# Kernel optimization log

Measured on AMD Instinct MI355X. Metric: run time of the kernel, lower is better.

The kernel has to match this reference:

```python
import jax, jax.numpy as jnp
import numpy as np

EPS = 1e-5

def _conv(x, w, b, groups=1, pad=0):
    # x: NCHW, w: OIHW (I = in_ch/groups)
    y = jax.lax.conv_general_dilated(
        x, w, window_strides=(1, 1), padding=[(pad, pad), (pad, pad)],
        feature_group_count=groups,
        dimension_numbers=('NCHW', 'OIHW', 'NCHW'))
    return y + b[None, :, None, None]

def _bn(x, g, b, m, v):
    scale = g * jax.lax.rsqrt(v + EPS)
    return x * scale[None, :, None, None] + (b - m * scale)[None, :, None, None]

def _block(x, w_dw, b_dw, w_pw, b_pw, g, b, m, v, groups):
    h = _conv(x, w_dw, b_dw, groups=groups, pad=1)   # 3x3 grouped conv
    h = _conv(h, w_pw, b_pw)                          # 1x1 pointwise 2C->C
    return jax.nn.relu(_bn(h, g, b, m, v))

def setup_inputs() -> dict:
    key = jax.random.key(0)
    ks = jax.random.split(key, 16)
    B, C, H, W = 4, 256, 64, 64
    s = 0.02  # small weight scale to keep softmax logits well-conditioned
    return {
        'x1': jax.random.normal(ks[0], (B, C, H, W), jnp.float32),
        'x2': jax.random.normal(ks[1], (B, C, H, W), jnp.float32),
        'w1_dw': jax.random.normal(ks[2], (2 * C, 2, 3, 3), jnp.float32) * s,
        'b1_dw': jnp.zeros((2 * C,), jnp.float32),
        'w1_pw': jax.random.normal(ks[3], (C, 2 * C, 1, 1), jnp.float32) * s,
        'b1_pw': jnp.zeros((C,), jnp.float32),
        'bn1_g': jnp.ones((C,), jnp.float32),
        'bn1_b': jnp.zeros((C,), jnp.float32),
        'bn1_m': jnp.zeros((C,), jnp.float32),
        'bn1_v': jnp.ones((C,), jnp.float32),
        'w2_dw': jax.random.normal(ks[4], (2 * C, 2, 3, 3), jnp.float32) * s,
        'b2_dw': jnp.zeros((2 * C,), jnp.float32),
        'w2_pw': jax.random.normal(ks[5], (C, 2 * C, 1, 1), jnp.float32) * s,
        'b2_pw': jnp.zeros((C,), jnp.float32),
        'bn2_g': jnp.ones((C,), jnp.float32),
        'bn2_b': jnp.zeros((C,), jnp.float32),
        'bn2_m': jnp.zeros((C,), jnp.float32),
        'bn2_v': jnp.ones((C,), jnp.float32),
        'wq': jax.random.normal(ks[6], (C // 8, C, 1, 1), jnp.float32) * s,
        'bq': jnp.zeros((C // 8,), jnp.float32),
        'wk': jax.random.normal(ks[7], (C // 8, C, 1, 1), jnp.float32) * s,
        'bk': jnp.zeros((C // 8,), jnp.float32),
        'wv': jax.random.normal(ks[8], (C, C, 1, 1), jnp.float32) * s,
        'bv': jnp.zeros((C,), jnp.float32),
        'gamma': jnp.ones((1,), jnp.float32),
    }

def reference(x1, x2,
              w1_dw, b1_dw, w1_pw, b1_pw, bn1_g, bn1_b, bn1_m, bn1_v,
              w2_dw, b2_dw, w2_pw, b2_pw, bn2_g, bn2_b, bn2_m, bn2_v,
              wq, bq, wk, bk, wv, bv, gamma):
    B, C, H, W = x1.shape
    N = H * W
    sub = x1 - x2
    concat1 = jnp.concatenate([sub, x1], axis=1)  # [B,2C,H,W]
    concat2 = jnp.concatenate([sub, x2], axis=1)
    x3 = _block(concat1, w1_dw, b1_dw, w1_pw, b1_pw, bn1_g, bn1_b, bn1_m, bn1_v, groups=C)
    x4 = _block(concat2, w2_dw, b2_dw, w2_pw, b2_pw, bn2_g, bn2_b, bn2_m, bn2_v, groups=C)
    q = _conv(x4, wq, bq).reshape(B, -1, N)   # [B, C//8, N]
    k = _conv(x3, wk, bk).reshape(B, -1, N)   # [B, C//8, N]
    v = _conv(x3, wv, bv).reshape(B, C, N)    # [B, C, N]
    energy = jnp.einsum('bdq,bdk->bqk', q, k)          # [B, N, N]
    attn = jax.nn.softmax(energy, axis=-1)
    out = jnp.einsum('bck,bqk->bcq', v, attn)          # [B, C, N]
    out = out.reshape(B, C, H, W)
    return gamma[0] * out + x1
```

## Files before the change

### kernel.cpp

```cpp
#include <hip/hip_runtime.h>
#include <hip/hip_bf16.h>

#define EPSB 1e-5f

typedef __hip_bfloat16 bf16;
typedef __attribute__((ext_vector_type(8))) short bf16x8;
typedef __attribute__((ext_vector_type(4))) float f32x4;

__device__ __forceinline__ unsigned short f2bu(float x) {
  bf16 h = __float2bfloat16(x);
  return *reinterpret_cast<unsigned short*>(&h);
}
__device__ __forceinline__ unsigned int pk2(float lo, float hi) {
  return ((unsigned int)f2bu(hi) << 16) | (unsigned int)f2bu(lo);
}

__global__ __launch_bounds__(256) void k_dwconv3(
    const float* __restrict__ x1, const float* __restrict__ x2,
    const float* __restrict__ w1, const float* __restrict__ b1,
    const float* __restrict__ w2, const float* __restrict__ b2,
    const float* __restrict__ w1pw, const float* __restrict__ w2pw,
    bf16* __restrict__ h1, bf16* __restrict__ h2,
    bf16* __restrict__ o1, bf16* __restrict__ o2) {
  if (blockIdx.y == 4) {
    int x = blockIdx.x;
    if (x < 128) {
      int i = (x * 256 + threadIdx.x) * 4;
      float4 a = *(const float4*)(w1pw + i);
      float4 c = *(const float4*)(w2pw + i);
      uint2 ua = {pk2(a.x, a.y), pk2(a.z, a.w)};
      uint2 uc = {pk2(c.x, c.y), pk2(c.z, c.w)};
      *(uint2*)&o1[i] = ua;
      *(uint2*)&o2[i] = uc;
    }
    return;
  }

  __shared__ float img[2 * 64 * 64];
  int g = blockIdx.x, b = blockIdx.y;
  int t = threadIdx.x;
  int row = t >> 2, x0 = (t & 3) * 16;
  bool xlo = (x0 == 0), xhi = (x0 == 48);
  size_t obase = (((size_t)(b * 512 + 2 * g)) << 12) + row * 64 + x0;

  auto stencil = [&](const float* wp, float bs0, float bs1, bf16* hout) {
    float o0[16], o1v[16];
#pragma unroll
    for (int i = 0; i < 16; i++) { o0[i] = bs0; o1v[i] = bs1; }
#pragma unroll
    for (int ch = 0; ch < 2; ch++) {
      float wa[9], wb[9];
#pragma unroll
      for (int i = 0; i < 9; i++) { wa[i] = wp[ch * 9 + i]; wb[i] = wp[18 + ch * 9 + i]; }
      const float* ib = img + ch * 4096;
#pragma unroll
      for (int ky = 0; ky < 3; ky++) {
        int yy = row + ky - 1;
        if (yy < 0 || yy > 63) continue;
        const float* rp = ib + yy * 64 + x0;
        float v[18];
        v[0] = xlo ? 0.f : rp[-1];
#pragma unroll
        for (int c = 1; c < 17; c++) v[c] = rp[c - 1];
        v[17] = xhi ? 0.f : rp[16];
        float a0 = wa[ky * 3], a1 = wa[ky * 3 + 1], a2 = wa[ky * 3 + 2];
        float c0 = wb[ky * 3], c1 = wb[ky * 3 + 1], c2 = wb[ky * 3 + 2];
#pragma unroll
        for (int i = 0; i < 16; i++) {
          o0[i] += a0 * v[i] + a1 * v[i + 1] + a2 * v[i + 2];
          o1v[i] += c0 * v[i] + c1 * v[i + 1] + c2 * v[i + 2];
        }
      }
    }
    uint4 u0 = {pk2(o0[0], o0[1]), pk2(o0[2], o0[3]), pk2(o0[4], o0[5]), pk2(o0[6], o0[7])};
    uint4 u1 = {pk2(o0[8], o0[9]), pk2(o0[10], o0[11]), pk2(o0[12], o0[13]), pk2(o0[14], o0[15])};
    *(uint4*)&hout[obase] = u0;
    *(uint4*)&hout[obase + 8] = u1;
    uint4 w0 = {pk2(o1v[0], o1v[1]), pk2(o1v[2], o1v[3]), pk2(o1v[4], o1v[5]), pk2(o1v[6], o1v[7])};
    uint4 w1v = {pk2(o1v[8], o1v[9]), pk2(o1v[10], o1v[11]), pk2(o1v[12], o1v[13]), pk2(o1v[14], o1v[15])};
    *(uint4*)&hout[obase + 4096] = w0;
    *(uint4*)&hout[obase + 4096 + 8] = w1v;
  };

  if (g < 128) {
    const float4* p1 = (const float4*)(x1 + ((size_t)(b * 256 + 2 * g) << 12));
    const float4* p2 = (const float4*)(x2 + ((size_t)(b * 256 + 2 * g) << 12));
#pragma unroll
    for (int u = 0; u < 8; u++) {
      int i = u * 256 + t;
      float4 a = p1[i], c = p2[i];
      float4 d = {a.x - c.x, a.y - c.y, a.z - c.z, a.w - c.w};
      ((float4*)img)[i] = d;
    }
  } else {
    const float4* p1 = (const float4*)(x1 + ((size_t)(b * 256 + 2 * (g - 128)) << 12));
#pragma unroll
    for (int u = 0; u < 8; u++) {
      int i = u * 256 + t;
      ((float4*)img)[i] = p1[i];
    }
  }
  __syncthreads();
  stencil(w1 + (size_t)(2 * g) * 18, b1[2 * g], b1[2 * g + 1], h1);

  if (g >= 128) {
    __syncthreads();
    const float4* p2 = (const float4*)(x2 + ((size_t)(b * 256 + 2 * (g - 128)) << 12));
#pragma unroll
    for (int u = 0; u < 8; u++) {
      int i = u * 256 + t;
      ((float4*)img)[i] = p2[i];
    }
    __syncthreads();
  }
  stencil(w2 + (size_t)(2 * g) * 18, b2[2 * g], b2[2 * g + 1], h2);
}

__global__ __launch_bounds__(256) void k_gemm_pw2(
    const bf16* __restrict__ In1, const bf16* __restrict__ In2,
    const bf16* __restrict__ W1, const bf16* __restrict__ W2,
    const float* __restrict__ bias1, const float* __restrict__ bias2,
    const float* __restrict__ g1v, const float* __restrict__ be1,
    const float* __restrict__ m1v, const float* __restrict__ v1v,
    const float* __restrict__ g2v, const float* __restrict__ be2,
    const float* __restrict__ m2v, const float* __restrict__ v2v,
    bf16* __restrict__ Out1, bf16* __restrict__ Out2) {
  __shared__ __align__(16) bf16 Al[128][40];
  __shared__ __align__(16) bf16 Bl[128][40];

  int lin = (blockIdx.z * 2 + blockIdx.y) * 32 + blockIdx.x;
  int xcd = lin & 7, slot = lin >> 3;
  int sel = xcd >> 2, b = xcd & 3;
  int p0 = (slot & 31) * 128;
  int oc0 = (slot >> 5) * 128;

  const bf16* In    = sel ? In2 : In1;
  const bf16* W     = sel ? W2 : W1;
  const float* bias = sel ? bias2 : bias1;
  const float* bng  = sel ? g2v : g1v;
  const float* bnb  = sel ? be2 : be1;
  const float* bnm  = sel ? m2v : m1v;
  const float* bnv  = sel ? v2v : v1v;
  bf16* Out         = sel ? Out2 : Out1;

  int t = threadIdx.x;
  int w = t >> 6, lane = t & 63, l16 = lane & 15, quad = lane >> 4;
  int wr = w >> 1, wc = w & 1;
  const bf16* Inb = In + (size_t)b * 512 * 4096;

  f32x4 acc[4][4];
#pragma unroll
  for (int mi = 0; mi < 4; mi++)
#pragma unroll
    for (int nj = 0; nj < 4; nj++) acc[mi][nj] = (f32x4){0.f, 0.f, 0.f, 0.f};

  int ocl = t >> 1, kb = (t & 1) * 16;
  int sch = t >> 3, soct = sch >> 3, swi = sch & 7, spg = t & 7;

  for (int kc = 0; kc < 512; kc += 32) {
    __syncthreads();
    {
      const bf16* src = W + (size_t)(oc0 + ocl) * 512 + kc + kb;
      uint4 u0 = *(const uint4*)(src);
      uint4 u1 = *(const uint4*)(src + 8);
      *(uint4*)&Al[ocl][kb] = u0;
      *(uint4*)&Al[ocl][kb + 8] = u1;
    }
    {
      const bf16* src = Inb + (size_t)(kc + sch) * 4096 + p0 + spg * 16;
      uint4 qv0 = *(const uint4*)src;
      uint4 qv1 = *(const uint4*)(src + 8);
      const unsigned short* qs0 = (const unsigned short*)&qv0;
      const unsigned short* qs1 = (const unsigned short*)&qv1;
#pragma unroll
      for (int j = 0; j < 8; j++) {
        int pix = spg * 16 + j;
        int col = (((soct ^ (pix >> 3)) & 3) << 3) | swi;
        *(unsigned short*)&Bl[pix][col] = qs0[j];
      }
#pragma unroll
      for (int j = 0; j < 8; j++) {
        int pix = spg * 16 + 8 + j;
        int col = (((soct ^ (pix >> 3)) & 3) << 3) | swi;
        *(unsigned short*)&Bl[pix][col] = qs1[j];
      }
    }
    __syncthreads();
    bf16x8 af[4], bv[4];
#pragma unroll
    for (int mi = 0; mi < 4; mi++)
      af[mi] = *(const bf16x8*)&Al[wr * 64 + mi * 16 + l16][quad * 8];
#pragma unroll
    for (int nj = 0; nj < 4; nj++) {
      int s = (nj * 2 + (l16 >> 3)) & 3;
      bv[nj] = *(const bf16x8*)&Bl[wc * 64 + nj * 16 + l16][(quad ^ s) * 8];
    }
#pragma unroll
    for (int mi = 0; mi < 4; mi++)
#pragma unroll
      for (int nj = 0; nj < 4; nj++)
        acc[mi][nj] = __builtin_amdgcn_mfma_f32_16x16x32_bf16(
            af[mi], bv[nj], acc[mi][nj], 0, 0, 0);
  }

#pragma unroll
  for (int mi = 0; mi < 4; mi++) {
    int ocb = oc0 + wr * 64 + mi * 16 + quad * 4;
    float4 bs4 = *(const float4*)&bias[ocb];
    float4 g4 = *(const float4*)&bng[ocb];
    float4 b4 = *(const float4*)&bnb[ocb];
    float4 m4 = *(const float4*)&bnm[ocb];
    float4 v4 = *(const float4*)&bnv[ocb];
    float sc[4], sh[4];
    sc[0] = g4.x * rsqrtf(v4.x + EPSB); sh[0] = bs4.x * sc[0] + b4.x - m4.x * sc[0];
    sc[1] = g4.y * rsqrtf(v4.y + EPSB); sh[1] = bs4.y * sc[1] + b4.y - m4.y * sc[1];
    sc[2] = g4.z * rsqrtf(v4.z + EPSB); sh[2] = bs4.z * sc[2] + b4.z - m4.z * sc[2];
    sc[3] = g4.w * rsqrtf(v4.w + EPSB); sh[3] = bs4.w * sc[3] + b4.w - m4.w * sc[3];
#pragma unroll
    for (int nj = 0; nj < 4; nj++) {
      int p = p0 + wc * 64 + nj * 16 + l16;
#pragma unroll
      for (int r = 0; r < 4; r++) {
        float val = fmaxf(acc[mi][nj][r] * sc[r] + sh[r], 0.f);
        Out[(((size_t)(b * 256 + ocb + r)) << 12) + p] = __float2bfloat16(val);
      }
    }
  }
}

__global__ __launch_bounds__(256) void k_gemm_qkv(
    const bf16* __restrict__ x3, const bf16* __restrict__ x4,
    const float* __restrict__ wv, const float* __restrict__ bv,
    const float* __restrict__ wq, const float* __restrict__ wk,
    const float* __restrict__ bq, const float* __restrict__ bk,
    bf16* __restrict__ vvb, bf16* __restrict__ qbf, bf16* __restrict__ kbf) {
  __shared__ __align__(16) bf16 Al[128][40];
  __shared__ __align__(16) bf16 Bl[128][40];

  int lin = (blockIdx.z * 2 + blockIdx.y) * 96 + blockIdx.x;
  int xcd = lin & 7, slot = lin >> 3;
  int b = xcd >> 1;
  int idx = ((xcd & 1) * 96) + slot;
  int by = idx / 96;
  int bx = idx % 96;

  int t = threadIdx.x;
  int w = t >> 6, lane = t & 63, l16 = lane & 15, quad = lane >> 4;
  int sch = t >> 3, soct = sch >> 3, swi = sch & 7, spg = t & 7;

  if (bx < 64) {
    int wr = w >> 1, wc = w & 1;
    int p0 = bx * 64;
    int oc0 = by * 128;
    const bf16* Inb = x3 + (size_t)b * 256 * 4096;

    f32x4 acc[4][2];
#pragma unroll
    for (int mi = 0; mi < 4; mi++)
#pragma unroll
      for (int nj = 0; nj < 2; nj++) acc[mi][nj] = (f32x4){0.f, 0.f, 0.f, 0.f};

    int ocl = t >> 1, kb = (t & 1) * 16;

    for (int kc = 0; kc < 256; kc += 32) {
      __syncthreads();
      {
        const float* src = wv + (size_t)(oc0 + ocl) * 256 + kc + kb;
        float4 f0 = *(const float4*)(src);
        float4 f1 = *(const float4*)(src + 4);
        float4 f2 = *(const float4*)(src + 8);
        float4 f3 = *(const float4*)(src + 12);
        uint4 u0 = {pk2(f0.x, f0.y), pk2(f0.z, f0.w), pk2(f1.x, f1.y), pk2(f1.z, f1.w)};
        uint4 u1 = {pk2(f2.x, f2.y), pk2(f2.z, f2.w), pk2(f3.x, f3.y), pk2(f3.z, f3.w)};
        *(uint4*)&Al[ocl][kb] = u0;
        *(uint4*)&Al[ocl][kb + 8] = u1;
      }
      {
        const bf16* src = Inb + (size_t)(kc + sch) * 4096 + p0 + spg * 8;
        uint4 qv = *(const uint4*)src;
        const unsigned short* qs = (const unsigned short*)&qv;
#pragma unroll
        for (int j = 0; j < 8; j++) {
          int pix = spg * 8 + j;
          int col = (((soct ^ (pix >> 3)) & 3) << 3) | swi;
          *(unsigned short*)&Bl[pix][col] = qs[j];
        }
      }
      __syncthreads();
      bf16x8 af[4], bvv[2];
#pragma unroll
      for (int mi = 0; mi < 4; mi++)
        af[mi] = *(const bf16x8*)&Al[wr * 64 + mi * 16 + l16][quad * 8];
#pragma unroll
      for (int nj = 0; nj < 2; nj++) {
        int s = (nj * 2 + (l16 >> 3)) & 3;
        bvv[nj] = *(const bf16x8*)&Bl[wc * 32 + nj * 16 + l16][(quad ^ s) * 8];
      }
#pragma unroll
      for (int mi = 0; mi < 4; mi++)
#pragma unroll
        for (int nj = 0; nj < 2; nj++)
          acc[mi][nj] = __builtin_amdgcn_mfma_f32_16x16x32_bf16(
              af[mi], bvv[nj], acc[mi][nj], 0, 0, 0);
    }

#pragma unroll
    for (int mi = 0; mi < 4; mi++) {
      int ocb = oc0 + wr * 64 + mi * 16 + quad * 4;
      float4 bs4 = *(const float4*)&bv[ocb];
      float sh[4] = {bs4.x, bs4.y, bs4.z, bs4.w};
#pragma unroll
      for (int nj = 0; nj < 2; nj++) {
        int p = p0 + wc * 32 + nj * 16 + l16;
#pragma unroll
        for (int r = 0; r < 4; r++) {
          float val = acc[mi][nj][r] + sh[r];
          vvb[(((size_t)(b * 256 + ocb + r)) << 12) + p] = __float2bfloat16(val);
        }
      }
    }
  } else {
    int p0 = (bx - 64) * 128;
    const bf16* In  = (by == 0) ? x4 : x3;
    const float* W  = (by == 0) ? wq : wk;
    const float* bi = (by == 0) ? bq : bk;
    bf16* Out       = (by == 0) ? qbf : kbf;
    const bf16* Inb = In + (size_t)b * 256 * 4096;

    f32x4 acc[2][2];
#pragma unroll
    for (int mi = 0; mi < 2; mi++)
#pragma unroll
      for (int nj = 0; nj < 2; nj++) acc[mi][nj] = (f32x4){0.f, 0.f, 0.f, 0.f};

    int aocl = t >> 3, akb = (t & 7) * 4;

    for (int kc = 0; kc < 256; kc += 32) {
      __syncthreads();
      {
        const float* src = W + (size_t)aocl * 256 + kc + akb;
        float4 f0 = *(const float4*)(src);
        uint2 u = {pk2(f0.x, f0.y), pk2(f0.z, f0.w)};
        *(uint2*)&Al[aocl][akb] = u;
      }
      {
        const bf16* src = Inb + (size_t)(kc + sch) * 4096 + p0 + spg * 16;
        uint4 qv0 = *(const uint4*)src;
        uint4 qv1 = *(const uint4*)(src + 8);
        const unsigned short* qs0 = (const unsigned short*)&qv0;
        const unsigned short* qs1 = (const unsigned short*)&qv1;
#pragma unroll
        for (int j = 0; j < 8; j++) {
          int pix = spg * 16 + j;
          int col = (((soct ^ (pix >> 3)) & 3) << 3) | swi;
          *(unsigned short*)&Bl[pix][col] = qs0[j];
        }
#pragma unroll
        for (int j = 0; j < 8; j++) {
          int pix = spg * 16 + 8 + j;
          int col = (((soct ^ (pix >> 3)) & 3) << 3) | swi;
          *(unsigned short*)&Bl[pix][col] = qs1[j];
        }
      }
      __syncthreads();
      bf16x8 af[2], bvv[2];
#pragma unroll
      for (int mi = 0; mi < 2; mi++)
        af[mi] = *(const bf16x8*)&Al[mi * 16 + l16][quad * 8];
#pragma unroll
      for (int nj = 0; nj < 2; nj++) {
        int s = (nj * 2 + (l16 >> 3)) & 3;
        bvv[nj] = *(const bf16x8*)&Bl[w * 32 + nj * 16 + l16][(quad ^ s) * 8];
      }
#pragma unroll
      for (int mi = 0; mi < 2; mi++)
#pragma unroll
        for (int nj = 0; nj < 2; nj++)
          acc[mi][nj] = __builtin_amdgcn_mfma_f32_16x16x32_bf16(
              af[mi], bvv[nj], acc[mi][nj], 0, 0, 0);
    }

#pragma unroll
    for (int mi = 0; mi < 2; mi++) {
      int ocb = mi * 16 + quad * 4;
      float4 bs4 = *(const float4*)&bi[ocb];
      float bs[4] = {bs4.x, bs4.y, bs4.z, bs4.w};
#pragma unroll
      for (int nj = 0; nj < 2; nj++) {
        int p = p0 + w * 32 + nj * 16 + l16;
        float v0 = acc[mi][nj][0] + bs[0];
        float v1 = acc[mi][nj][1] + bs[1];
        float v2 = acc[mi][nj][2] + bs[2];
        float v3 = acc[mi][nj][3] + bs[3];
        uint2 u = {pk2(v0, v1), pk2(v2, v3)};
        *(uint2*)&Out[((size_t)(b * 4096) + p) * 32 + ocb] = u;
      }
    }
  }
}

__global__ __launch_bounds__(512, 4) void k_attn_mfma(
    const bf16* __restrict__ qb, const bf16* __restrict__ kb,
    const bf16* __restrict__ vb, const float* __restrict__ x1,
    const float* __restrict__ gamma, float* __restrict__ out) {
  __shared__ __align__(16) bf16 Pl[2][64 * 128];
  __shared__ float lsumw[8][64];

  int t = threadIdx.x;
  int w = t >> 6, lane = t & 63;
  int l16 = lane & 15, quad = lane >> 4;

  int lin = blockIdx.y * 128 + blockIdx.x;
  int xcd = lin & 7, slot = lin >> 3;
  int b = xcd >> 1;
  int chalf = xcd & 1;
  int q0 = slot * 64;

  const bf16* kbb = kb + (size_t)b * 4096 * 32;
  const bf16* vbb = vb + ((size_t)(b * 256 + chalf * 128)) * 4096;

  bf16x8 qf[4];
#pragma unroll
  for (int nj = 0; nj < 4; nj++)
    qf[nj] = *(const bf16x8*)(qb + ((size_t)(b * 4096 + q0 + nj * 16 + l16)) * 32 + quad * 8);

  f32x4 acc[4];
#pragma unroll
  for (int nj = 0; nj < 4; nj++) acc[nj] = (f32x4){0.f, 0.f, 0.f, 0.f};
  float lpart[4] = {0.f, 0.f, 0.f, 0.f};

  const bf16* kptr = kbb + ((size_t)(w * 16 + l16)) * 32 + quad * 8;
  const bf16* vptr = vbb + ((size_t)(w * 16 + l16)) * 4096 + quad * 8;

  int c16w = w * 2 + (quad >> 1);
  int off8 = (quad & 1) * 4;

  auto load_kv = [&](int j0, bf16x8& kf, bf16x8 vf[4]) {
    kf = *(const bf16x8*)(kptr + (size_t)j0 * 32);
#pragma unroll
    for (int kc = 0; kc < 4; kc++)
      vf[kc] = *(const bf16x8*)(vptr + j0 + kc * 32);
  };

  auto s_phase = [&](const bf16x8& kf, int pb) {
    bf16* P = Pl[pb];
    __builtin_amdgcn_s_setprio(1);
#pragma unroll
    for (int nj = 0; nj < 4; nj++) {
      f32x4 s = __builtin_amdgcn_mfma_f32_16x16x32_bf16(
          kf, qf[nj], (f32x4){0.f, 0.f, 0.f, 0.f}, 0, 0, 0);
      float p0f = __expf(fminf(s[0], 80.f));
      float p1f = __expf(fminf(s[1], 80.f));
      float p2f = __expf(fminf(s[2], 80.f));
      float p3f = __expf(fminf(s[3], 80.f));
      lpart[nj] += (p0f + p1f) + (p2f + p3f);
      int row = nj * 16 + l16;
      int c16 = c16w ^ (row & 15);
      uint2 u = {pk2(p0f, p1f), pk2(p2f, p3f)};
      *(uint2*)&P[row * 128 + c16 * 8 + off8] = u;
    }
    __builtin_amdgcn_s_setprio(0);
  };

  auto pv_phase = [&](const bf16x8 vf[4], int pb) {
    const bf16* P = Pl[pb];
#pragma unroll
    for (int kc = 0; kc < 4; kc++) {
      bf16x8 pf[4];
#pragma unroll
      for (int nj = 0; nj < 4; nj++) {
        int row = nj * 16 + l16;
        int c16 = (kc * 4 + quad) ^ (row & 15);
        pf[nj] = *(const bf16x8*)&P[row * 128 + c16 * 8];
      }
      __builtin_amdgcn_s_setprio(1);
#pragma unroll
      for (int nj = 0; nj < 4; nj++)
        acc[nj] = __builtin_amdgcn_mfma_f32_16x16x32_bf16(
            vf[kc], pf[nj], acc[nj], 0, 0, 0);
      __builtin_amdgcn_s_setprio(0);
    }
  };

  bf16x8 kfA, kfB, vfA[4], vfB[4];
  load_kv(0, kfA, vfA);
  s_phase(kfA, 0);

  for (int i = 0; i < 32; i += 2) {
    __syncthreads();
    if (i < 31) load_kv((i + 1) * 128, kfB, vfB);
    pv_phase(vfA, 0);
    if (i < 31) s_phase(kfB, 1);
    __syncthreads();
    if (i + 2 < 32) load_kv((i + 2) * 128, kfA, vfA);
    if (i + 1 < 32) pv_phase(vfB, 1);
    if (i + 2 < 32) s_phase(kfA, 0);
  }

#pragma unroll
  for (int nj = 0; nj < 4; nj++) {
    float v = lpart[nj];
    v += __shfl_xor(v, 16);
    v += __shfl_xor(v, 32);
    lpart[nj] = v;
  }
  if (lane < 16) {
#pragma unroll
    for (int nj = 0; nj < 4; nj++) lsumw[w][nj * 16 + lane] = lpart[nj];
  }
  __syncthreads();

  float gm = gamma[0];
#pragma unroll
  for (int nj = 0; nj < 4; nj++) {
    int ql = nj * 16 + l16;
    float ls = 0.f;
#pragma unroll
    for (int w8 = 0; w8 < 8; w8++) ls += lsumw[w8][ql];
    float gl = gm / ls;
    int cb = chalf * 128 + w * 16 + quad * 4;
#pragma unroll
    for (int r = 0; r < 4; r++) {
      size_t gidx = (((size_t)(b * 256 + cb + r)) << 12) + q0 + ql;
      out[gidx] = gl * acc[nj][r] + x1[gidx];
    }
  }
}

extern "C" void kernel_launch(void* const* d_in, const int* in_sizes, int n_in,
                              void* d_out, int out_size, void* d_ws, size_t ws_size,
                              hipStream_t stream) {
  const float* x1    = (const float*)d_in[0];
  const float* x2    = (const float*)d_in[1];
  const float* w1_dw = (const float*)d_in[2];
  const float* b1_dw = (const float*)d_in[3];
  const float* w1_pw = (const float*)d_in[4];
  const float* b1_pw = (const float*)d_in[5];
  const float* bn1_g = (const float*)d_in[6];
  const float* bn1_b = (const float*)d_in[7];
  const float* bn1_m = (const float*)d_in[8];
  const float* bn1_v = (const float*)d_in[9];
  const float* w2_dw = (const float*)d_in[10];
  const float* b2_dw = (const float*)d_in[11];
  const float* w2_pw = (const float*)d_in[12];
  const float* b2_pw = (const float*)d_in[13];
  const float* bn2_g = (const float*)d_in[14];
  const float* bn2_b = (const float*)d_in[15];
  const float* bn2_m = (const float*)d_in[16];
  const float* bn2_v = (const float*)d_in[17];
  const float* wq    = (const float*)d_in[18];
  const float* bq    = (const float*)d_in[19];
  const float* wk    = (const float*)d_in[20];
  const float* bk    = (const float*)d_in[21];
  const float* wv    = (const float*)d_in[22];
  const float* bv    = (const float*)d_in[23];
  const float* gamma = (const float*)d_in[24];

  bf16* wsb = (bf16*)d_ws;
  bf16* h1  = wsb;
  bf16* h2  = wsb + 8388608;
  bf16* x3  = wsb + 16777216;
  bf16* x4  = wsb + 20971520;
  bf16* qbf = wsb + 25165824;
  bf16* kbf = wsb + 25690112;
  bf16* vvb = wsb + 26214400;
  bf16* w1b = vvb;
  bf16* w2b = vvb + 131072;

  k_dwconv3<<<dim3(256, 5), 256, 0, stream>>>(x1, x2, w1_dw, b1_dw, w2_dw, b2_dw,
                                              w1_pw, w2_pw, h1, h2, w1b, w2b);
  k_gemm_pw2<<<dim3(32, 2, 8), 256, 0, stream>>>(h1, h2, w1b, w2b, b1_pw, b2_pw,
                                                 bn1_g, bn1_b, bn1_m, bn1_v,
                                                 bn2_g, bn2_b, bn2_m, bn2_v, x3, x4);
  k_gemm_qkv<<<dim3(96, 2, 4), 256, 0, stream>>>(x3, x4, wv, bv, wq, wk, bq, bk,
                                                 vvb, qbf, kbf);
  k_attn_mfma<<<dim3(128, 4), 512, 0, stream>>>(qbf, kbf, vvb, x1, gamma, (float*)d_out);
}
```

Before: 261.2 us.

## Deepen pointwise GEMM K-step, widen V-projection tiles, drop exp clamp

```diff
diff --git a/kernel.cpp b/kernel.cpp
--- a/kernel.cpp
+++ b/kernel.cpp
@@ -125,8 +125,8 @@
     const float* __restrict__ g2v, const float* __restrict__ be2,
     const float* __restrict__ m2v, const float* __restrict__ v2v,
     bf16* __restrict__ Out1, bf16* __restrict__ Out2) {
-  __shared__ __align__(16) bf16 Al[128][40];
-  __shared__ __align__(16) bf16 Bl[128][40];
+  __shared__ __align__(16) bf16 Al[128][72];
+  __shared__ __align__(16) bf16 Bl[128][72];
 
   int lin = (blockIdx.z * 2 + blockIdx.y) * 32 + blockIdx.x;
   int xcd = lin & 7, slot = lin >> 3;
@@ -154,53 +154,54 @@
 #pragma unroll
     for (int nj = 0; nj < 4; nj++) acc[mi][nj] = (f32x4){0.f, 0.f, 0.f, 0.f};
 
-  int ocl = t >> 1, kb = (t & 1) * 16;
-  int sch = t >> 3, soct = sch >> 3, swi = sch & 7, spg = t & 7;
-
-  for (int kc = 0; kc < 512; kc += 32) {
+  int ocl = t >> 1, kb = (t & 1) * 32;
+  int sch = t >> 2, soct = sch >> 3, swi = sch & 7, spg4 = t & 3;
+
+  for (int kc = 0; kc < 512; kc += 64) {
     __syncthreads();
     {
       const bf16* src = W + (size_t)(oc0 + ocl) * 512 + kc + kb;
       uint4 u0 = *(const uint4*)(src);
       uint4 u1 = *(const uint4*)(src + 8);
+      uint4 u2 = *(const uint4*)(src + 16);
+      uint4 u3 = *(const uint4*)(src + 24);
       *(uint4*)&Al[ocl][kb] = u0;
       *(uint4*)&Al[ocl][kb + 8] = u1;
+      *(uint4*)&Al[ocl][kb + 16] = u2;
+      *(uint4*)&Al[ocl][kb + 24] = u3;
     }
     {
-      const bf16* src = Inb + (size_t)(kc + sch) * 4096 + p0 + spg * 16;
-      uint4 qv0 = *(const uint4*)src;
-      uint4 qv1 = *(const uint4*)(src + 8);
-      const unsigned short* qs0 = (const unsigned short*)&qv0;
-      const unsigned short* qs1 = (const unsigned short*)&qv1;
-#pragma unroll
-      for (int j = 0; j < 8; j++) {
-        int pix = spg * 16 + j;
-        int col = (((soct ^ (pix >> 3)) & 3) << 3) | swi;
-        *(unsigned short*)&Bl[pix][col] = qs0[j];
-      }
-#pragma unroll
-      for (int j = 0; j < 8; j++) {
-        int pix = spg * 16 + 8 + j;
-        int col = (((soct ^ (pix >> 3)) & 3) << 3) | swi;
-        *(unsigned short*)&Bl[pix][col] = qs1[j];
+      const bf16* src = Inb + (size_t)(kc + sch) * 4096 + p0 + spg4 * 32;
+#pragma unroll
+      for (int u = 0; u < 4; u++) {
+        uint4 qv = *(const uint4*)(src + u * 8);
+        const unsigned short* qs = (const unsigned short*)&qv;
+        int pixb = spg4 * 32 + u * 8;
+        int col = (((soct ^ (pixb >> 3)) & 7) << 3) | swi;
+#pragma unroll
+        for (int j = 0; j < 8; j++)
+          *(unsigned short*)&Bl[pixb + j][col] = qs[j];
       }
     }
     __syncthreads();
-    bf16x8 af[4], bv[4];
-#pragma unroll
-    for (int mi = 0; mi < 4; mi++)
-      af[mi] = *(const bf16x8*)&Al[wr * 64 + mi * 16 + l16][quad * 8];
-#pragma unroll
-    for (int nj = 0; nj < 4; nj++) {
-      int s = (nj * 2 + (l16 >> 3)) & 3;
-      bv[nj] = *(const bf16x8*)&Bl[wc * 64 + nj * 16 + l16][(quad ^ s) * 8];
-    }
-#pragma unroll
-    for (int mi = 0; mi < 4; mi++)
-#pragma unroll
-      for (int nj = 0; nj < 4; nj++)
-        acc[mi][nj] = __builtin_amdgcn_mfma_f32_16x16x32_bf16(
-            af[mi], bv[nj], acc[mi][nj], 0, 0, 0);
+#pragma unroll
+    for (int h = 0; h < 2; h++) {
+      bf16x8 af[4], bv[4];
+#pragma unroll
+      for (int mi = 0; mi < 4; mi++)
+        af[mi] = *(const bf16x8*)&Al[wr * 64 + mi * 16 + l16][h * 32 + quad * 8];
+#pragma unroll
+      for (int nj = 0; nj < 4; nj++) {
+        int s = (nj * 2 + (l16 >> 3)) & 7;
+        bv[nj] = *(const bf16x8*)&Bl[wc * 64 + nj * 16 + l16][(((h * 4 + quad) ^ s) & 7) * 8];
+      }
+#pragma unroll
+      for (int mi = 0; mi < 4; mi++)
+#pragma unroll
+        for (int nj = 0; nj < 4; nj++)
+          acc[mi][nj] = __builtin_amdgcn_mfma_f32_16x16x32_bf16(
+              af[mi], bv[nj], acc[mi][nj], 0, 0, 0);
+    }
   }
 
 #pragma unroll
@@ -237,28 +238,28 @@
   __shared__ __align__(16) bf16 Al[128][40];
   __shared__ __align__(16) bf16 Bl[128][40];
 
-  int lin = (blockIdx.z * 2 + blockIdx.y) * 96 + blockIdx.x;
+  int lin = (blockIdx.z * 2 + blockIdx.y) * 64 + blockIdx.x;
   int xcd = lin & 7, slot = lin >> 3;
   int b = xcd >> 1;
-  int idx = ((xcd & 1) * 96) + slot;
-  int by = idx / 96;
-  int bx = idx % 96;
+  int idx = ((xcd & 1) * 64) + slot;
+  int by = idx >> 6;
+  int bx = idx & 63;
 
   int t = threadIdx.x;
   int w = t >> 6, lane = t & 63, l16 = lane & 15, quad = lane >> 4;
   int sch = t >> 3, soct = sch >> 3, swi = sch & 7, spg = t & 7;
 
-  if (bx < 64) {
+  if (bx < 32) {
     int wr = w >> 1, wc = w & 1;
-    int p0 = bx * 64;
+    int p0 = bx * 128;
     int oc0 = by * 128;
     const bf16* Inb = x3 + (size_t)b * 256 * 4096;
 
-    f32x4 acc[4][2];
+    f32x4 acc[4][4];
 #pragma unroll
     for (int mi = 0; mi < 4; mi++)
 #pragma unroll
-      for (int nj = 0; nj < 2; nj++) acc[mi][nj] = (f32x4){0.f, 0.f, 0.f, 0.f};
+      for (int nj = 0; nj < 4; nj++) acc[mi][nj] = (f32x4){0.f, 0.f, 0.f, 0.f};
 
     int ocl = t >> 1, kb = (t & 1) * 16;
 
@@ -276,30 +277,38 @@
         *(uint4*)&Al[ocl][kb + 8] = u1;
       }
       {
-        const bf16* src = Inb + (size_t)(kc + sch) * 4096 + p0 + spg * 8;
-        uint4 qv = *(const uint4*)src;
-        const unsigned short* qs = (const unsigned short*)&qv;
+        const bf16* src = Inb + (size_t)(kc + sch) * 4096 + p0 + spg * 16;
+        uint4 qv0 = *(const uint4*)src;
+        uint4 qv1 = *(const uint4*)(src + 8);
+        const unsigned short* qs0 = (const unsigned short*)&qv0;
+        const unsigned short* qs1 = (const unsigned short*)&qv1;
 #pragma unroll
         for (int j = 0; j < 8; j++) {
-          int pix = spg * 8 + j;
+          int pix = spg * 16 + j;
           int col = (((soct ^ (pix >> 3)) & 3) << 3) | swi;
-          *(unsigned short*)&Bl[pix][col] = qs[j];
+          *(unsigned short*)&Bl[pix][col] = qs0[j];
         }
+#pragma unroll
+        for (int j = 0; j < 8; j++) {
+          int pix = spg * 16 + 8 + j;
+          int col = (((soct ^ (pix >> 3)) & 3) << 3) | swi;
+          *(unsigned short*)&Bl[pix][col] = qs1[j];
+        }
       }
       __syncthreads();
-      bf16x8 af[4], bvv[2];
+      bf16x8 af[4], bvv[4];
 #pragma unroll
       for (int mi = 0; mi < 4; mi++)
         af[mi] = *(const bf16x8*)&Al[wr * 64 + mi * 16 + l16][quad * 8];
 #pragma unroll
-      for (int nj = 0; nj < 2; nj++) {
+      for (int nj = 0; nj < 4; nj++) {
         int s = (nj * 2 + (l16 >> 3)) & 3;
-        bvv[nj] = *(const bf16x8*)&Bl[wc * 32 + nj * 16 + l16][(quad ^ s) * 8];
+        bvv[nj] = *(const bf16x8*)&Bl[wc * 64 + nj * 16 + l16][(quad ^ s) * 8];
       }
 #pragma unroll
       for (int mi = 0; mi < 4; mi++)
 #pragma unroll
-        for (int nj = 0; nj < 2; nj++)
+        for (int nj = 0; nj < 4; nj++)
           acc[mi][nj] = __builtin_amdgcn_mfma_f32_16x16x32_bf16(
               af[mi], bvv[nj], acc[mi][nj], 0, 0, 0);
     }
@@ -310,8 +319,8 @@
       float4 bs4 = *(const float4*)&bv[ocb];
       float sh[4] = {bs4.x, bs4.y, bs4.z, bs4.w};
 #pragma unroll
-      for (int nj = 0; nj < 2; nj++) {
-        int p = p0 + wc * 32 + nj * 16 + l16;
+      for (int nj = 0; nj < 4; nj++) {
+        int p = p0 + wc * 64 + nj * 16 + l16;
 #pragma unroll
         for (int r = 0; r < 4; r++) {
           float val = acc[mi][nj][r] + sh[r];
@@ -320,7 +329,7 @@
       }
     }
   } else {
-    int p0 = (bx - 64) * 128;
+    int p0 = (bx - 32) * 128;
     const bf16* In  = (by == 0) ? x4 : x3;
     const float* W  = (by == 0) ? wq : wk;
     const float* bi = (by == 0) ? bq : bk;
@@ -449,10 +458,10 @@
     for (int nj = 0; nj < 4; nj++) {
       f32x4 s = __builtin_amdgcn_mfma_f32_16x16x32_bf16(
           kf, qf[nj], (f32x4){0.f, 0.f, 0.f, 0.f}, 0, 0, 0);
-      float p0f = __expf(fminf(s[0], 80.f));
-      float p1f = __expf(fminf(s[1], 80.f));
-      float p2f = __expf(fminf(s[2], 80.f));
-      float p3f = __expf(fminf(s[3], 80.f));
+      float p0f = __expf(s[0]);
+      float p1f = __expf(s[1]);
+      float p2f = __expf(s[2]);
+      float p3f = __expf(s[3]);
       lpart[nj] += (p0f + p1f) + (p2f + p3f);
       int row = nj * 16 + l16;
       int c16 = c16w ^ (row & 15);
@@ -572,7 +581,7 @@
   k_gemm_pw2<<<dim3(32, 2, 8), 256, 0, stream>>>(h1, h2, w1b, w2b, b1_pw, b2_pw,
                                                  bn1_g, bn1_b, bn1_m, bn1_v,
                                                  bn2_g, bn2_b, bn2_m, bn2_v, x3, x4);
-  k_gemm_qkv<<<dim3(96, 2, 4), 256, 0, stream>>>(x3, x4, wv, bv, wq, wk, bq, bk,
+  k_gemm_qkv<<<dim3(64, 2, 4), 256, 0, stream>>>(x3, x4, wv, bv, wq, wk, bq, bk,
                                                  vvb, qbf, kbf);
   k_attn_mfma<<<dim3(128, 4), 512, 0, stream>>>(qbf, kbf, vvb, x1, gamma, (float*)d_out);
 }
```

After: 255.4 us. 1.02x faster.
